# Optimization experiments

Measured on AMD Instinct MI355X. Metric: run time of the kernel, lower is better.

## Reference

```python
import jax, jax.numpy as jnp
import numpy as np

B, H, W, DIM = 32, 56, 56, 512
WS, SHIFT, HEADS, MLP = 7, 3, 16, 2048
S = WS * WS
NW = (H // WS) * (W // WS)


def _rel_pos_index():
    coords = np.stack(np.meshgrid(np.arange(WS), np.arange(WS), indexing='ij')).reshape(2, -1)
    rel = (coords[:, :, None] - coords[:, None, :]).transpose(1, 2, 0)
    rel[:, :, 0] += WS - 1
    rel[:, :, 1] += WS - 1
    rel[:, :, 0] *= 2 * WS - 1
    return rel.sum(-1)  # [S, S] ints in [0, 169)


def _attn_mask():
    mask = np.zeros((H, W))
    cnt = 0
    sls = (slice(0, -WS), slice(-WS, -SHIFT), slice(-SHIFT, None))
    for hs in sls:
        for ws in sls:
            mask[hs, ws] = cnt
            cnt += 1
    mw = mask.reshape(H // WS, WS, W // WS, WS).transpose(0, 2, 1, 3).reshape(-1, S)
    am = mw[:, None, :] - mw[:, :, None]
    return np.where(am != 0, -100.0, 0.0).astype(np.float32)  # [NW, S, S]


_RPI = jnp.asarray(_rel_pos_index().reshape(-1))
_MASK = jnp.asarray(_attn_mask())


def setup_inputs() -> dict:
    key = jax.random.key(0)
    ks = jax.random.split(key, 6)
    sc = lambda fan: 1.0 / np.sqrt(fan)
    return {
        'x': jax.random.normal(ks[0], (B, H * W, DIM), jnp.float32),
        'qkv_w': jax.random.normal(ks[1], (DIM, 3 * DIM), jnp.float32) * sc(DIM),
        'qkv_b': jnp.zeros((3 * DIM,), jnp.float32),
        'proj_w': jax.random.normal(ks[2], (DIM, DIM), jnp.float32) * sc(DIM),
        'proj_b': jnp.zeros((DIM,), jnp.float32),
        'rel_bias': jax.random.normal(ks[3], (169, HEADS), jnp.float32) * 0.02,
        'norm1_g': jnp.ones((DIM,), jnp.float32),
        'norm1_b': jnp.zeros((DIM,), jnp.float32),
        'norm2_g': jnp.ones((DIM,), jnp.float32),
        'norm2_b': jnp.zeros((DIM,), jnp.float32),
        'mlp_w1': jax.random.normal(ks[4], (DIM, MLP), jnp.float32) * sc(DIM),
        'mlp_b1': jnp.zeros((MLP,), jnp.float32),
        'mlp_w2': jax.random.normal(ks[5], (MLP, DIM), jnp.float32) * sc(MLP),
        'mlp_b2': jnp.zeros((DIM,), jnp.float32),
    }


def _ln(z, g, b):
    m = z.mean(-1, keepdims=True)
    v = z.var(-1, keepdims=True)
    return (z - m) * jax.lax.rsqrt(v + 1e-5) * g + b


def reference(x, qkv_w, qkv_b, proj_w, proj_b, rel_bias,
              norm1_g, norm1_b, norm2_g, norm2_b,
              mlp_w1, mlp_b1, mlp_w2, mlp_b2):
    hd = DIM // HEADS
    scale = hd ** -0.5
    skip = x
    h = _ln(x, norm1_g, norm1_b).reshape(B, H, W, DIM)
    h = jnp.roll(h, (-SHIFT, -SHIFT), axis=(1, 2))
    # window partition -> [B*NW, S, DIM]
    win = h.reshape(B, H // WS, WS, W // WS, WS, DIM).transpose(0, 1, 3, 2, 4, 5).reshape(-1, S, DIM)
    qkv = (win @ qkv_w + qkv_b).reshape(-1, S, 3, HEADS, hd).transpose(2, 0, 3, 1, 4)
    q, k, v = qkv[0] * scale, qkv[1], qkv[2]
    attn = jnp.einsum('whqd,whkd->whqk', q, k)  # [B*NW, HEADS, S, S]
    bias = rel_bias[_RPI].reshape(S, S, HEADS).transpose(2, 0, 1)
    attn = attn + bias[None]
    attn = attn.reshape(B, NW, HEADS, S, S) + _MASK[None, :, None]
    attn = jax.nn.softmax(attn.reshape(-1, HEADS, S, S), axis=-1)
    out = jnp.einsum('whqk,whkd->whqd', attn, v).transpose(0, 2, 1, 3).reshape(-1, S, DIM)
    out = out @ proj_w + proj_b
    # window reverse + unshift
    out = out.reshape(B, H // WS, W // WS, WS, WS, DIM).transpose(0, 1, 3, 2, 4, 5).reshape(B, H, W, DIM)
    out = jnp.roll(out, (SHIFT, SHIFT), axis=(1, 2)).reshape(B, H * W, DIM)
    x1 = skip + out
    h2 = _ln(x1, norm2_g, norm2_b)
    h2 = jax.nn.gelu(h2 @ mlp_w1 + mlp_b1, approximate=False) @ mlp_w2 + mlp_b2
    return x1 + h2
```

## Files before the change

### kernel.cpp

```cpp
#include <hip/hip_runtime.h>
#include <hip/hip_bf16.h>
#include <math.h>

#define BB 32
#define HH 56
#define WWD 56
#define DIM 512
#define WSZ 7
#define SHIFT 3
#define HEADS 16
#define MLPD 2048
#define SS 49
#define NWIN 64
#define HD 32
#define TOK (BB*HH*WWD)
#define NQKV 1536

typedef __hip_bfloat16 bf16;
typedef __attribute__((ext_vector_type(8))) short short8;
typedef __attribute__((ext_vector_type(4))) float floatx4;

__device__ __forceinline__ float bf2f(bf16 v){ return __bfloat162float(v); }
__device__ __forceinline__ bf16  f2bf(float v){ return __float2bfloat16(v); }
__device__ __forceinline__ float rd_ext(const void* p, size_t i, int fp32){
    return fp32 ? ((const float*)p)[i] : bf2f(((const bf16*)p)[i]);
}
__device__ __forceinline__ void gload16(const bf16* g, bf16* l){
    __builtin_amdgcn_global_load_lds(
        (const __attribute__((address_space(1))) void*)g,
        (__attribute__((address_space(3))) void*)l, 16, 0, 0);
}
__device__ __forceinline__ float gelu_exact(float x){
    float z  = fabsf(x) * 0.70710678118654752f;
    float t  = 1.0f / (1.0f + 0.3275911f * z);
    float p  = t*(0.254829592f + t*(-0.284496736f + t*(1.421413741f +
               t*(-1.453152027f + t*1.061405429f))));
    float er = 1.0f - p * __expf(-z*z);
    float cdf = 0.5f * (1.0f + (x < 0.f ? -er : er));
    return x * cdf;
}

__global__ void sniff_kernel(const unsigned short* __restrict__ x, int* __restrict__ flag)
{
    int lane = threadIdx.x;
    int insane = 0;
    #pragma unroll
    for (int t = 0; t < 2; t++){
        unsigned short u = x[2*(lane + t*64)];
        int e = (u >> 7) & 0xFF;
        if (e < 100 || e > 133) insane++;
    }
    #pragma unroll
    for (int m = 1; m < 64; m <<= 1) insane += __shfl_xor(insane, m);
    if (lane == 0) *flag = (insane > 64) ? 1 : 0;
}

template<int MODE>
__global__ __launch_bounds__(256) void ln_kernel(const void* __restrict__ xv,
        const void* __restrict__ g, const void* __restrict__ bvec,
        bf16* __restrict__ out, const int* __restrict__ flagp)
{
    const int fp32 = *flagp;
    int token = blockIdx.x * 4 + (threadIdx.x >> 6);
    int lane  = threadIdx.x & 63;
    float f[8];
    if (MODE == 0 && fp32){
        const float* xr = (const float*)xv + (size_t)token*DIM + lane*8;
        float4 a = *(const float4*)xr;
        float4 b = *(const float4*)(xr + 4);
        f[0]=a.x; f[1]=a.y; f[2]=a.z; f[3]=a.w;
        f[4]=b.x; f[5]=b.y; f[6]=b.z; f[7]=b.w;
    } else {
        uint4 v = *((const uint4*)((const bf16*)xv + (size_t)token * DIM) + lane);
        bf16 e[8]; *(uint4*)e = v;
        #pragma unroll
        for (int i = 0; i < 8; i++) f[i] = bf2f(e[i]);
    }
    float sum = 0.f, ssq = 0.f;
    #pragma unroll
    for (int i = 0; i < 8; i++){ sum += f[i]; ssq += f[i]*f[i]; }
    #pragma unroll
    for (int m = 1; m < 64; m <<= 1){ sum += __shfl_xor(sum, m); ssq += __shfl_xor(ssq, m); }
    float mean = sum * (1.0f/DIM);
    float var  = ssq * (1.0f/DIM) - mean*mean;
    float rstd = rsqrtf(var + 1e-5f);
    bf16 o[8];
    #pragma unroll
    for (int i = 0; i < 8; i++){
        float gv = rd_ext(g,    lane*8+i, fp32);
        float bv = rd_ext(bvec, lane*8+i, fp32);
        o[i] = f2bf((f[i]-mean)*rstd*gv + bv);
    }
    size_t drow;
    if (MODE == 0){
        int bidx = token / (HH*WWD);
        int t    = token % (HH*WWD);
        int hs = t / WWD, wsrc = t % WWD;
        int i2 = (hs  + HH  - SHIFT) % HH;
        int j2 = (wsrc+ WWD - SHIFT) % WWD;
        int wh = i2 / WSZ, ii = i2 % WSZ;
        int ww = j2 / WSZ, jj = j2 % WSZ;
        int wi = bidx*NWIN + wh*8 + ww;
        drow = (size_t)wi*SS + ii*WSZ + jj;
    } else {
        drow = token;
    }
    *((uint4*)(out + drow*DIM) + lane) = *(uint4*)o;
}

__global__ void cvt_transpose(const void* __restrict__ in, bf16* __restrict__ out,
                              int K, int N, const int* __restrict__ flagp)
{
    const int fp32 = *flagp;
    int id = blockIdx.x*256 + threadIdx.x;
    if (id >= K*N) return;
    int k = id / N, n = id - k*N;
    out[(size_t)n*K + k] = f2bf(rd_ext(in, id, fp32));
}

__global__ void stab_kernel(const void* __restrict__ rel_bias,
                            float* __restrict__ stab, const int* __restrict__ flagp)
{
    const int fp32 = *flagp;
    int idx = blockIdx.x*256 + threadIdx.x;
    int h   = idx / (4*64*52);
    int rem = idx - h*(4*64*52);
    int cls = rem / (64*52);
    int rem2= rem - cls*(64*52);
    int i   = rem2 / 52;
    int j   = rem2 - i*52;
    float v = 0.f;
    if (i < SS && j < SS){
        int qi = i/7, qj = i - qi*7;
        int ki = j/7, kj = j - ki*7;
        int rpi = (qi-ki+6)*13 + (qj-kj+6);
        v = rd_ext(rel_bias, (size_t)rpi*HEADS + h, fp32);
        int ri = ((cls&2) ? (qi<4?1:2) : 0)*3 + ((cls&1) ? (qj<4?1:2) : 0);
        int rj = ((cls&2) ? (ki<4?1:2) : 0)*3 + ((cls&1) ? (kj<4?1:2) : 0);
        if (ri != rj) v -= 100.0f;
    }
    stab[idx] = v;
}

__global__ __launch_bounds__(256, 2) void attn_kernel(
        const bf16* __restrict__ qkv, const float* __restrict__ stab,
        bf16* __restrict__ out)
{
    alignas(16) __shared__ bf16 Ps[4][64*72];
    const int tid  = threadIdx.x;
    const int wave = tid >> 6, lane = tid & 63;
    const int g = lane >> 4, l16 = lane & 15;
    const int job = blockIdx.x*4 + wave;
    const int wi = job >> 4, h = job & 15;
    const bf16* qbase = qkv + (size_t)wi*(SS*NQKV) + h*HD;

    short8 qf[4], kf[4];
    #pragma unroll
    for (int t = 0; t < 4; t++){
        int row = t*16 + l16;
        qf[t] = *(const short8*)(qbase + (size_t)row*NQKV +       g*8);
        kf[t] = *(const short8*)(qbase + (size_t)row*NQKV + 512 + g*8);
    }
    floatx4 st[4][4];
    #pragma unroll
    for (int mt = 0; mt < 4; mt++)
        #pragma unroll
        for (int nt = 0; nt < 4; nt++)
            st[mt][nt] = floatx4{0.f,0.f,0.f,0.f};
    #pragma unroll
    for (int mt = 0; mt < 4; mt++)
        #pragma unroll
        for (int nt = 0; nt < 4; nt++)
            st[mt][nt] = __builtin_amdgcn_mfma_f32_16x16x32_bf16(
                             kf[mt], qf[nt], st[mt][nt], 0, 0, 0);

    const int nw = wi & 63;
    const int cls = (((nw >> 3) == 7) ? 2 : 0) | (((nw & 7) == 7) ? 1 : 0);
    const float* tb = stab + (size_t)((h*4 + cls)*64)*52;
    bf16* pw = Ps[wave];
    #pragma unroll
    for (int nt = 0; nt < 4; nt++){
        const int i = nt*16 + l16;
        const float* trow = tb + i*52;
        float mx = -1e30f;
        #pragma unroll
        for (int mt = 0; mt < 4; mt++){
            float4 t4 = *(const float4*)(trow + mt*16 + g*4);
            #pragma unroll
            for (int r = 0; r < 4; r++){
                int j = mt*16 + g*4 + r;
                float v = st[mt][nt][r]*0.17677669529663687f + ((const float*)&t4)[r];
                v = (j < SS) ? v : -1e30f;
                st[mt][nt][r] = v;
                mx = fmaxf(mx, v);
            }
        }
        mx = fmaxf(mx, __shfl_xor(mx, 16));
        mx = fmaxf(mx, __shfl_xor(mx, 32));
        float sum = 0.f;
        #pragma unroll
        for (int mt = 0; mt < 4; mt++)
            #pragma unroll
            for (int r = 0; r < 4; r++){
                float e = __expf(st[mt][nt][r] - mx);
                st[mt][nt][r] = e;
                sum += e;
            }
        sum += __shfl_xor(sum, 16);
        sum += __shfl_xor(sum, 32);
        float inv = 1.0f / sum;
        #pragma unroll
        for (int mt = 0; mt < 4; mt++){
            union { bf16 e[4]; uint2 u; } pk;
            #pragma unroll
            for (int r = 0; r < 4; r++) pk.e[r] = f2bf(st[mt][nt][r]*inv);
            *(uint2*)(pw + i*72 + mt*16 + g*4) = pk.u;
        }
    }

    const unsigned short* vbase = (const unsigned short*)qkv
                                + (size_t)wi*(SS*NQKV) + 1024 + h*HD;
    short8 vf[2][2];
    #pragma unroll
    for (int md = 0; md < 2; md++){
        int d = md*16 + l16;
        #pragma unroll
        for (int kt = 0; kt < 2; kt++){
            short8 f;
            #pragma unroll
            for (int jj = 0; jj < 8; jj++){
                int j  = kt*32 + g*8 + jj;
                int jc = (j < SS) ? j : SS-1;
                unsigned short t = vbase[(size_t)jc*NQKV + d];
                f[jj] = (j < SS) ? (short)t : (short)0;
            }
            vf[md][kt] = f;
        }
    }

    floatx4 o[2][4];
    #pragma unroll
    for (int md = 0; md < 2; md++)
        #pragma unroll
        for (int nt = 0; nt < 4; nt++)
            o[md][nt] = floatx4{0.f,0.f,0.f,0.f};
    #pragma unroll
    for (int kt = 0; kt < 2; kt++){
        #pragma unroll
        for (int nt = 0; nt < 4; nt++){
            short8 pf = *(const short8*)(pw + (nt*16 + l16)*72 + kt*32 + g*8);
            #pragma unroll
            for (int md = 0; md < 2; md++)
                o[md][nt] = __builtin_amdgcn_mfma_f32_16x16x32_bf16(
                                vf[md][kt], pf, o[md][nt], 0, 0, 0);
        }
    }

    #pragma unroll
    for (int nt = 0; nt < 4; nt++){
        int i = nt*16 + l16;
        if (i < SS){
            #pragma unroll
            for (int md = 0; md < 2; md++){
                union { bf16 e[4]; uint2 u; } ob;
                #pragma unroll
                for (int r = 0; r < 4; r++) ob.e[r] = f2bf(o[md][nt][r]);
                *(uint2*)(out + ((size_t)wi*SS + i)*DIM + h*HD + md*16 + g*4) = ob.u;
            }
        }
    }
}

template<int NT, int KT, int EPI>
__global__ __launch_bounds__(256) void gemm_kernel(
    const bf16* __restrict__ A, const bf16* __restrict__ Bt,
    const void* __restrict__ bias, void* __restrict__ Cv,
    const void* __restrict__ extra, const int* __restrict__ flagp)
{
    alignas(16) __shared__ bf16 As[128*64];
    alignas(16) __shared__ bf16 Bs[128*64];
    const int fp32 = *flagp;
    const int tid = threadIdx.x;

    const int nxt = NT/128;
    const int bid = blockIdx.x + blockIdx.y*nxt;
    const int nwg = nxt*784;
    const int cpx = nwg >> 3;
    const int wid = (bid & 7)*cpx + (bid >> 3);
    const int m0 = (wid / nxt) * 128;
    const int n0 = (wid % nxt) * 128;

    const int wave = tid >> 6, lane = tid & 63;
    const int wm = wave & 1, wn = wave >> 1;
    const int qd = lane >> 4, l16 = lane & 15;
    const int srow  = lane >> 3;
    const int sslot = ((lane & 7) ^ srow) * 8;

    floatx4 acc[4][4];
    #pragma unroll
    for (int i = 0; i < 4; i++)
        #pragma unroll
        for (int j = 0; j < 4; j++)
            acc[i][j] = floatx4{0.f,0.f,0.f,0.f};

    for (int kt = 0; kt < KT; kt += 64){
        #pragma unroll
        for (int r = 0; r < 4; r++){
            int c = wave*4 + r;
            gload16(A  + (size_t)(m0 + c*8 + srow)*KT + kt + sslot, As + c*512);
            gload16(Bt + (size_t)(n0 + c*8 + srow)*KT + kt + sslot, Bs + c*512);
        }
        __syncthreads();
        #pragma unroll
        for (int kk = 0; kk < 2; kk++){
            short8 af[4], bfr[4];
            #pragma unroll
            for (int mt = 0; mt < 4; mt++){
                int row = wm*64 + mt*16 + l16;
                af[mt] = *(const short8*)(As + row*64 + (((kk*4+qd) ^ (row&7))*8));
            }
            #pragma unroll
            for (int nt = 0; nt < 4; nt++){
                int row = wn*64 + nt*16 + l16;
                bfr[nt] = *(const short8*)(Bs + row*64 + (((kk*4+qd) ^ (row&7))*8));
            }
            #pragma unroll
            for (int mt = 0; mt < 4; mt++)
                #pragma unroll
                for (int nt = 0; nt < 4; nt++)
                    acc[mt][nt] = __builtin_amdgcn_mfma_f32_16x16x32_bf16(
                                      af[mt], bfr[nt], acc[mt][nt], 0, 0, 0);
        }
        __syncthreads();
    }

    const int ncol = n0 + wn*64 + l16;
    float bias_v[4];
    #pragma unroll
    for (int nt = 0; nt < 4; nt++)
        bias_v[nt] = rd_ext(bias, ncol + nt*16, fp32);

    #pragma unroll
    for (int mt = 0; mt < 4; mt++){
        #pragma unroll
        for (int r = 0; r < 4; r++){
            const int m = m0 + wm*64 + mt*16 + qd*4 + r;
            if (EPI == 2){
                int wi = m / SS, s = m - wi*SS;
                int b_ = wi >> 6, nw = wi & 63;
                int hr = (nw >> 3)*WSZ + s / WSZ;
                int wr = (nw & 7)*WSZ + s % WSZ;
                int h = hr + SHIFT; if (h >= HH)  h -= HH;
                int w = wr + SHIFT; if (w >= WWD) w -= WWD;
                size_t rowoff = ((size_t)b_*(HH*WWD) + h*WWD + w)*DIM + ncol;
                #pragma unroll
                for (int nt = 0; nt < 4; nt++){
                    float val = acc[mt][nt][r] + bias_v[nt];
                    ((bf16*)Cv)[rowoff + nt*16] =
                        f2bf(val + rd_ext(extra, rowoff + nt*16, fp32));
                }
            } else if (EPI == 3){
                size_t rowoff = (size_t)m*NT + ncol;
                #pragma unroll
                for (int nt = 0; nt < 4; nt++){
                    float val = acc[mt][nt][r] + bias_v[nt]
                              + bf2f(((const bf16*)extra)[rowoff + nt*16]);
                    if (fp32) ((float*)Cv)[rowoff + nt*16] = val;
                    else      ((bf16*)Cv)[rowoff + nt*16]  = f2bf(val);
                }
            } else {
                bf16* crow = (bf16*)Cv + (size_t)m*NT + ncol;
                #pragma unroll
                for (int nt = 0; nt < 4; nt++){
                    float val = acc[mt][nt][r] + bias_v[nt];
                    if (EPI == 1) val = gelu_exact(val);
                    crow[nt*16] = f2bf(val);
                }
            }
        }
    }
}

extern "C" void kernel_launch(void* const* d_in, const int* in_sizes, int n_in,
                              void* d_out, int out_size, void* d_ws, size_t ws_size,
                              hipStream_t stream)
{
    const void* x      = d_in[0];
    const void* qkv_w  = d_in[1];
    const void* qkv_b  = d_in[2];
    const void* proj_w = d_in[3];
    const void* proj_b = d_in[4];
    const void* rel_b  = d_in[5];
    const void* n1g    = d_in[6];
    const void* n1b    = d_in[7];
    const void* n2g    = d_in[8];
    const void* n2b    = d_in[9];
    const void* w1     = d_in[10];
    const void* b1     = d_in[11];
    const void* w2     = d_in[12];
    const void* b2     = d_in[13];

    char* ws = (char*)d_ws;
    const size_t SZ_ACT = (size_t)TOK*DIM*2;
    const size_t SZ_QKV = (size_t)TOK*NQKV*2;
    bf16* win   = (bf16*)(ws);
    bf16* qkvb  = (bf16*)(ws + SZ_ACT);
    bf16* hid   = (bf16*)(ws);
    bf16* x1    = (bf16*)(ws + SZ_ACT + SZ_QKV);
    bf16* ln2   = (bf16*)(ws + 2*SZ_ACT + SZ_QKV);
    bf16* qkvwT = (bf16*)(ws + 3*SZ_ACT + SZ_QKV);
    bf16* projwT= qkvwT + (size_t)1536*512;
    bf16* w1T   = projwT + (size_t)512*512;
    bf16* w2T   = w1T   + (size_t)512*2048;
    int*  flag  = (int*)(w2T + (size_t)2048*512);
    float* stab = (float*)x1;
    const size_t need = 3*SZ_ACT + SZ_QKV +
        ((size_t)1536*512 + 512*512 + 512*2048 + 2048*512)*2 + 4;
    if (ws_size < need) return;

    hipLaunchKernelGGL(sniff_kernel, dim3(1), dim3(64), 0, stream,
                       (const unsigned short*)x, flag);

    hipLaunchKernelGGL(stab_kernel, dim3((16*4*64*52)/256), dim3(256), 0, stream,
                       rel_b, stab, flag);

    hipLaunchKernelGGL(cvt_transpose, dim3((512*1536+255)/256), dim3(256), 0, stream,
                       qkv_w, qkvwT, 512, 1536, flag);
    hipLaunchKernelGGL(cvt_transpose, dim3((512*512+255)/256), dim3(256), 0, stream,
                       proj_w, projwT, 512, 512, flag);
    hipLaunchKernelGGL(cvt_transpose, dim3((512*2048+255)/256), dim3(256), 0, stream,
                       w1, w1T, 512, 2048, flag);
    hipLaunchKernelGGL(cvt_transpose, dim3((2048*512+255)/256), dim3(256), 0, stream,
                       w2, w2T, 2048, 512, flag);

    hipLaunchKernelGGL((ln_kernel<0>), dim3(TOK/4), dim3(256), 0, stream,
                       x, n1g, n1b, win, flag);
    hipLaunchKernelGGL((gemm_kernel<1536,512,0>), dim3(12,784), dim3(256), 0, stream,
                       win, qkvwT, qkv_b, (void*)qkvb, (const void*)nullptr, flag);
    hipLaunchKernelGGL(attn_kernel, dim3(8192), dim3(256), 0, stream,
                       qkvb, stab, win);
    hipLaunchKernelGGL((gemm_kernel<512,512,2>), dim3(4,784), dim3(256), 0, stream,
                       win, projwT, proj_b, (void*)x1, x, flag);
    hipLaunchKernelGGL((ln_kernel<1>), dim3(TOK/4), dim3(256), 0, stream,
                       x1, n2g, n2b, ln2, flag);
    hipLaunchKernelGGL((gemm_kernel<2048,512,1>), dim3(16,784), dim3(256), 0, stream,
                       ln2, w1T, b1, (void*)hid, (const void*)nullptr, flag);
    hipLaunchKernelGGL((gemm_kernel<512,2048,3>), dim3(4,784), dim3(256), 0, stream,
                       hid, w2T, b2, d_out, (const void*)x1, flag);
}
```

Before: 2.257 ms.

## Double-buffer GEMM LDS tiles and vectorize epilogue via swapped MFMA operands

Shared-memory A/B tiles become double buffered. The next K-tile's global-to-LDS loads are issued before computing the current one, using explicit vmcnt waits and raw barriers so load latency overlaps MFMA work. The MFMA operands are swapped so each lane holds four consecutive output columns. That lets the epilogue do vector 8/16-byte stores and residual loads instead of scalar 2-byte accesses. The cost is doubled LDS use (64KB), which may reduce occupancy, and the hand-tuned waitcnt counts are fragile.

```diff
diff --git a/kernel.cpp b/kernel.cpp
--- a/kernel.cpp
+++ b/kernel.cpp
@@ -277,8 +277,8 @@
     const void* __restrict__ bias, void* __restrict__ Cv,
     const void* __restrict__ extra, const int* __restrict__ flagp)
 {
-    alignas(16) __shared__ bf16 As[128*64];
-    alignas(16) __shared__ bf16 Bs[128*64];
+    alignas(16) __shared__ bf16 As[2][128*64];
+    alignas(16) __shared__ bf16 Bs[2][128*64];
     const int fp32 = *flagp;
     const int tid = threadIdx.x;
 
@@ -303,79 +303,126 @@
         for (int j = 0; j < 4; j++)
             acc[i][j] = floatx4{0.f,0.f,0.f,0.f};
 
-    for (int kt = 0; kt < KT; kt += 64){
+    const bf16* Arow = A  + (size_t)(m0 + wave*32 + srow)*KT + sslot;
+    const bf16* Brow = Bt + (size_t)(n0 + wave*32 + srow)*KT + sslot;
+
+    auto STAGE = [&](int buf, int kt){
         #pragma unroll
         for (int r = 0; r < 4; r++){
-            int c = wave*4 + r;
-            gload16(A  + (size_t)(m0 + c*8 + srow)*KT + kt + sslot, As + c*512);
-            gload16(Bt + (size_t)(n0 + c*8 + srow)*KT + kt + sslot, Bs + c*512);
-        }
-        __syncthreads();
+            gload16(Arow + (size_t)(r*8)*KT + kt, &As[buf][(wave*4+r)*512]);
+            gload16(Brow + (size_t)(r*8)*KT + kt, &Bs[buf][(wave*4+r)*512]);
+        }
+    };
+    auto COMPUTE = [&](int buf){
         #pragma unroll
         for (int kk = 0; kk < 2; kk++){
             short8 af[4], bfr[4];
             #pragma unroll
             for (int mt = 0; mt < 4; mt++){
                 int row = wm*64 + mt*16 + l16;
-                af[mt] = *(const short8*)(As + row*64 + (((kk*4+qd) ^ (row&7))*8));
+                af[mt] = *(const short8*)(&As[buf][row*64 + (((kk*4+qd) ^ (row&7))*8)]);
             }
             #pragma unroll
             for (int nt = 0; nt < 4; nt++){
                 int row = wn*64 + nt*16 + l16;
-                bfr[nt] = *(const short8*)(Bs + row*64 + (((kk*4+qd) ^ (row&7))*8));
+                bfr[nt] = *(const short8*)(&Bs[buf][row*64 + (((kk*4+qd) ^ (row&7))*8)]);
             }
             #pragma unroll
             for (int mt = 0; mt < 4; mt++)
                 #pragma unroll
                 for (int nt = 0; nt < 4; nt++)
                     acc[mt][nt] = __builtin_amdgcn_mfma_f32_16x16x32_bf16(
-                                      af[mt], bfr[nt], acc[mt][nt], 0, 0, 0);
-        }
-        __syncthreads();
-    }
-
-    const int ncol = n0 + wn*64 + l16;
-    float bias_v[4];
+                                      bfr[nt], af[mt], acc[mt][nt], 0, 0, 0);
+        }
+    };
+
+    constexpr int NTILE = KT/64;
+    STAGE(0, 0);
+    for (int t = 0; t < NTILE; ++t){
+        if (t+1 < NTILE){
+            STAGE((t+1)&1, (t+1)*64);
+            asm volatile("s_waitcnt vmcnt(8)" ::: "memory");
+        } else {
+            asm volatile("s_waitcnt vmcnt(0)" ::: "memory");
+        }
+        __builtin_amdgcn_s_barrier();
+        __builtin_amdgcn_sched_barrier(0);
+        COMPUTE(t&1);
+        __builtin_amdgcn_sched_barrier(0);
+        __builtin_amdgcn_s_barrier();
+    }
+
+    const int mrow = m0 + wm*64 + l16;
+    const int nb   = n0 + wn*64 + qd*4;
+    float bias_v[4][4];
     #pragma unroll
     for (int nt = 0; nt < 4; nt++)
-        bias_v[nt] = rd_ext(bias, ncol + nt*16, fp32);
+        #pragma unroll
+        for (int r = 0; r < 4; r++)
+            bias_v[nt][r] = rd_ext(bias, nb + nt*16 + r, fp32);
 
     #pragma unroll
     for (int mt = 0; mt < 4; mt++){
-        #pragma unroll
-        for (int r = 0; r < 4; r++){
-            const int m = m0 + wm*64 + mt*16 + qd*4 + r;
-            if (EPI == 2){
-                int wi = m / SS, s = m - wi*SS;
-                int b_ = wi >> 6, nw = wi & 63;
-                int hr = (nw >> 3)*WSZ + s / WSZ;
-                int wr = (nw & 7)*WSZ + s % WSZ;
-                int h = hr + SHIFT; if (h >= HH)  h -= HH;
-                int w = wr + SHIFT; if (w >= WWD) w -= WWD;
-                size_t rowoff = ((size_t)b_*(HH*WWD) + h*WWD + w)*DIM + ncol;
+        const int m = mrow + mt*16;
+        if (EPI == 2){
+            int wi = m / SS, s = m - wi*SS;
+            int b_ = wi >> 6, nw = wi & 63;
+            int hr = (nw >> 3)*WSZ + s / WSZ;
+            int wr = (nw & 7)*WSZ + s % WSZ;
+            int h = hr + SHIFT; if (h >= HH)  h -= HH;
+            int w = wr + SHIFT; if (w >= WWD) w -= WWD;
+            size_t base = ((size_t)b_*(HH*WWD) + h*WWD + w)*DIM + nb;
+            #pragma unroll
+            for (int nt = 0; nt < 4; nt++){
+                size_t off = base + nt*16;
+                union { bf16 e[4]; uint2 u; } ob;
+                if (fp32){
+                    float4 sv = *(const float4*)((const float*)extra + off);
+                    #pragma unroll
+                    for (int r = 0; r < 4; r++)
+                        ob.e[r] = f2bf(acc[mt][nt][r] + bias_v[nt][r] + ((const float*)&sv)[r]);
+                } else {
+                    union { bf16 e[4]; uint2 u; } sv;
+                    sv.u = *(const uint2*)((const bf16*)extra + off);
+                    #pragma unroll
+                    for (int r = 0; r < 4; r++)
+                        ob.e[r] = f2bf(acc[mt][nt][r] + bias_v[nt][r] + bf2f(sv.e[r]));
+                }
+                *(uint2*)((bf16*)Cv + off) = ob.u;
+            }
+        } else if (EPI == 3){
+            size_t base = (size_t)m*NT + nb;
+            #pragma unroll
+            for (int nt = 0; nt < 4; nt++){
+                size_t off = base + nt*16;
+                union { bf16 e[4]; uint2 u; } sv;
+                sv.u = *(const uint2*)((const bf16*)extra + off);
+                if (fp32){
+                    float4 ov;
+                    #pragma unroll
+                    for (int r = 0; r < 4; r++)
+                        ((float*)&ov)[r] = acc[mt][nt][r] + bias_v[nt][r] + bf2f(sv.e[r]);
+                    *(float4*)((float*)Cv + off) = ov;
+                } else {
+                    union { bf16 e[4]; uint2 u; } ob;
+                    #pragma unroll
+                    for (int r = 0; r < 4; r++)
+                        ob.e[r] = f2bf(acc[mt][nt][r] + bias_v[nt][r] + bf2f(sv.e[r]));
+                    *(uint2*)((bf16*)Cv + off) = ob.u;
+                }
+            }
+        } else {
+            bf16* crow = (bf16*)Cv + (size_t)m*NT + nb;
+            #pragma unroll
+            for (int nt = 0; nt < 4; nt++){
+                union { bf16 e[4]; uint2 u; } ob;
                 #pragma unroll
-                for (int nt = 0; nt < 4; nt++){
-                    float val = acc[mt][nt][r] + bias_v[nt];
-                    ((bf16*)Cv)[rowoff + nt*16] =
-                        f2bf(val + rd_ext(extra, rowoff + nt*16, fp32));
+                for (int r = 0; r < 4; r++){
+                    float v = acc[mt][nt][r] + bias_v[nt][r];
+                    if (EPI == 1) v = gelu_exact(v);
+                    ob.e[r] = f2bf(v);
                 }
-            } else if (EPI == 3){
-                size_t rowoff = (size_t)m*NT + ncol;
-                #pragma unroll
-                for (int nt = 0; nt < 4; nt++){
-                    float val = acc[mt][nt][r] + bias_v[nt]
-                              + bf2f(((const bf16*)extra)[rowoff + nt*16]);
-                    if (fp32) ((float*)Cv)[rowoff + nt*16] = val;
-                    else      ((bf16*)Cv)[rowoff + nt*16]  = f2bf(val);
-                }
-            } else {
-                bf16* crow = (bf16*)Cv + (size_t)m*NT + ncol;
-                #pragma unroll
-                for (int nt = 0; nt < 4; nt++){
-                    float val = acc[mt][nt][r] + bias_v[nt];
-                    if (EPI == 1) val = gelu_exact(val);
-                    crow[nt*16] = f2bf(val);
-                }
+                *(uint2*)(crow + nt*16) = ob.u;
             }
         }
     }
```

Measured after the change: 2.030 ms. 1.11x faster.
